# Performance work log

Hardware: AMD Instinct MI355X
Metric: run time of the kernel (lower is better)

The kernel has to match this reference:

```python
import jax, jax.numpy as jnp
import numpy as np

B, S, E, H = 4, 2048, 1024, 16
D = E // H
EPS = 1e-6


def setup_inputs() -> dict:
    key = jax.random.key(0)
    ks = jax.random.split(key, 6)
    glorot = lambda k: jax.random.uniform(k, (E, E), jnp.float32,
                                          -np.sqrt(6.0 / (E + E)), np.sqrt(6.0 / (E + E)))
    return {
        "x": jax.random.normal(ks[0], (B, S, E), jnp.float32),
        "mask": jnp.zeros((B, 1, 1, S), jnp.float32),
        "Wq": glorot(ks[1]), "bq": jnp.zeros((E,), jnp.float32),
        "Wk": glorot(ks[2]), "bk": jnp.zeros((E,), jnp.float32),
        "Wv": glorot(ks[3]), "bv": jnp.zeros((E,), jnp.float32),
        "Wo": glorot(ks[4]), "bo": jnp.zeros((E,), jnp.float32),
        "gamma": jnp.ones((E,), jnp.float32),
        "beta": jnp.zeros((E,), jnp.float32),
    }


def _split_heads(t):
    # [B, S, E] -> [B, H, S, D]
    return t.reshape(B, S, H, D).transpose(0, 2, 1, 3)


def reference(x, mask, Wq, bq, Wk, bk, Wv, bv, Wo, bo, gamma, beta):
    q = _split_heads(x @ Wq + bq)
    k = _split_heads(x @ Wk + bk)
    v = _split_heads(x @ Wv + bv)
    # NOTE: original divides by sqrt(embedding_size), not sqrt(depth)
    scores = jnp.einsum("bhqd,bhkd->bhqk", q, k) / jnp.sqrt(jnp.float32(E))
    scores = scores + mask * (-1e9)
    attn = jax.nn.softmax(scores, axis=-1)
    ctx = jnp.einsum("bhqk,bhkd->bhqd", attn, v)
    ctx = ctx.transpose(0, 2, 1, 3).reshape(B, S, E)
    main_out = ctx @ Wo + bo
    # dropout is identity (is_training=False); residual is the raw input
    added = main_out + x
    mu = jnp.mean(added, axis=-1, keepdims=True)
    var = jnp.mean(jnp.square(added - mu), axis=-1, keepdims=True)
    return gamma * (added - mu) / jnp.sqrt(var + EPS) + beta
```

## Files before the change

### kernel.cpp

```cpp
#include <hip/hip_runtime.h>
#include <hip/hip_bf16.h>


typedef __bf16 bf16_t;
typedef __bf16 bf16x8 __attribute__((ext_vector_type(8)));
typedef __bf16 bf16x4v __attribute__((ext_vector_type(4)));
typedef float f32x4 __attribute__((ext_vector_type(4)));

#define LDS_AS __attribute__((address_space(3)))
#define GLB_AS __attribute__((address_space(1)))

__device__ __forceinline__ void async16(bf16_t* lds, const bf16_t* g) {
  __builtin_amdgcn_global_load_lds((GLB_AS void*)const_cast<bf16_t*>(g),
                                   (LDS_AS void*)lds, 16, 0, 0);
}

__device__ __forceinline__ f32x4 mfma16(bf16x8 a, bf16x8 b, f32x4 c) {
  return __builtin_amdgcn_mfma_f32_16x16x32_bf16(a, b, c, 0, 0, 0);
}

__device__ __forceinline__ float fast_exp2(float x) {
#if __has_builtin(__builtin_amdgcn_exp2f)
  return __builtin_amdgcn_exp2f(x);
#else
  return __expf(x * 0.6931471805599453f);
#endif
}

__global__ __launch_bounds__(256) void prep_k(
    const float* __restrict__ w0, const float* __restrict__ w1,
    const float* __restrict__ w2, const float* __restrict__ w3,
    bf16_t* __restrict__ dst,
    const float* __restrict__ x, bf16_t* __restrict__ xb)
{
  const int tx = threadIdx.x, ty = threadIdx.y;
  if (blockIdx.z == 4) {
    const int id = (blockIdx.y * 32 + blockIdx.x) * 256 + ty * 32 + tx;
#pragma unroll
    for (int it = 0; it < 8; ++it) {
      const size_t i = ((size_t)id + (size_t)it * 262144) * 4;
      const float4 v = *(const float4*)(x + i);
      bf16x4v o;
      o[0] = (bf16_t)v.x; o[1] = (bf16_t)v.y; o[2] = (bf16_t)v.z; o[3] = (bf16_t)v.w;
      *(bf16x4v*)(xb + i) = o;
    }
    return;
  }
  __shared__ bf16_t tile[32][33];
  const float* src = (blockIdx.z == 0) ? w0 : (blockIdx.z == 1) ? w1
                   : (blockIdx.z == 2) ? w2 : w3;
  bf16_t* d = dst + (size_t)blockIdx.z * 1024 * 1024;
  const int bx = blockIdx.x * 32, by = blockIdx.y * 32;
#pragma unroll
  for (int r = 0; r < 32; r += 8)
    tile[ty + r][tx] = (bf16_t)src[(size_t)(by + ty + r) * 1024 + bx + tx];
  __syncthreads();
#pragma unroll
  for (int r = 0; r < 32; r += 8)
    d[(size_t)(bx + ty + r) * 1024 + by + tx] = tile[tx][ty + r];
}

__global__ __launch_bounds__(256) void gemm_qkv(
    const bf16_t* __restrict__ X, const bf16_t* __restrict__ WtAll,
    const float* __restrict__ bq, const float* __restrict__ bk,
    const float* __restrict__ bv,
    bf16_t* __restrict__ Qb, bf16_t* __restrict__ Kb, bf16_t* __restrict__ Vtb)
{
  __shared__ __align__(16) bf16_t As[128 * 64];
  __shared__ __align__(16) bf16_t Bs[128 * 64];

  const int z = blockIdx.z;
  const bf16_t* Bt = WtAll + (size_t)z * 1024 * 1024;
  const float* bias = (z == 0) ? bq : (z == 1) ? bk : bv;
  const int bm0 = blockIdx.x * 128;
  const int bn0 = blockIdx.y * 128;
  const int t = threadIdx.x;
  const int w = t >> 6, lane = t & 63;
  const int wm = w >> 1, wn = w & 1;
  const int l15 = lane & 15, quad = lane >> 4;
  const int srow8 = lane >> 3;
  const int sp8   = lane & 7;

  f32x4 acc[4][4] = {};

  for (int k0 = 0; k0 < 1024; k0 += 64) {
    __syncthreads();
#pragma unroll
    for (int i = 0; i < 4; ++i) {
      const int row = (w * 4 + i) * 8 + srow8;
      const int c = sp8 ^ (row & 7);
      async16(&As[row * 64 + sp8 * 8], X  + (size_t)(bm0 + row) * 1024 + k0 + c * 8);
      async16(&Bs[row * 64 + sp8 * 8], Bt + (size_t)(bn0 + row) * 1024 + k0 + c * 8);
    }
    __syncthreads();

    bf16x8 af[4][2], bfr[4][2];
#pragma unroll
    for (int mi = 0; mi < 4; ++mi) {
      const int r = wm * 64 + mi * 16 + l15;
#pragma unroll
      for (int kc = 0; kc < 2; ++kc) {
        const int pg = (kc * 4 + quad) ^ (r & 7);
        af[mi][kc] = *(const bf16x8*)&As[r * 64 + pg * 8];
      }
    }
#pragma unroll
    for (int ni = 0; ni < 4; ++ni) {
      const int r = wn * 64 + ni * 16 + l15;
#pragma unroll
      for (int kc = 0; kc < 2; ++kc) {
        const int pg = (kc * 4 + quad) ^ (r & 7);
        bfr[ni][kc] = *(const bf16x8*)&Bs[r * 64 + pg * 8];
      }
    }
#pragma unroll
    for (int kc = 0; kc < 2; ++kc)
#pragma unroll
      for (int mi = 0; mi < 4; ++mi)
#pragma unroll
        for (int ni = 0; ni < 4; ++ni)
          acc[mi][ni] = mfma16(af[mi][kc], bfr[ni][kc], acc[mi][ni]);
  }

  const float QSCALE = 0.045084220f;

#pragma unroll
  for (int ni = 0; ni < 4; ++ni) {
    const int n = bn0 + wn * 64 + ni * 16 + l15;
    const float bb = bias[n];
    const int h = n >> 6, dd = n & 63;
    if (z == 2) {
#pragma unroll
      for (int mi = 0; mi < 4; ++mi) {
        const int m0 = bm0 + wm * 64 + mi * 16 + quad * 4;
        const int bi = m0 >> 11, s = m0 & 2047;
        bf16x4v vk;
#pragma unroll
        for (int r = 0; r < 4; ++r) vk[r] = (bf16_t)(acc[mi][ni][r] + bb);
        *(bf16x4v*)&Vtb[((size_t)(bi * 16 + h) * 64 + dd) * 2048 + s] = vk;
      }
    } else {
#pragma unroll
      for (int mi = 0; mi < 4; ++mi) {
#pragma unroll
        for (int r = 0; r < 4; ++r) {
          const int m = bm0 + wm * 64 + mi * 16 + quad * 4 + r;
          const float v = acc[mi][ni][r] + bb;
          const int bi = m >> 11, s = m & 2047;
          if (z == 0)
            Qb[((size_t)(bi * 16 + h) * 2048 + s) * 64 + dd] = (bf16_t)(v * QSCALE);
          else
            Kb[((size_t)(bi * 16 + h) * 2048 + s) * 64 + dd] = (bf16_t)v;
        }
      }
    }
  }
}

__global__ __launch_bounds__(256) void attn_k(
    const bf16_t* __restrict__ Qb, const bf16_t* __restrict__ Kb,
    const bf16_t* __restrict__ Vtb, const float* __restrict__ mask,
    bf16_t* __restrict__ Ctx)
{
  __shared__ __align__(16) bf16_t Ks[2][64 * 64];
  __shared__ __align__(16) bf16_t Vs[2][64 * 64];
  __shared__ __align__(16) bf16_t Ps[256 * 64];

  const int qt = blockIdx.x, bh = blockIdx.y;
  const int bi = bh >> 4, h = bh & 15;
  const int q0 = qt * 256;
  const bf16_t* Qh = Qb + (size_t)bh * 2048 * 64;
  const bf16_t* Kh = Kb + (size_t)bh * 2048 * 64;
  const bf16_t* Vh = Vtb + (size_t)bh * 64 * 2048;
  const float* mrow = mask + (size_t)bi * 2048;

  const int t = threadIdx.x;
  const int w = t >> 6, lane = t & 63;
  const int l15 = lane & 15, quad = lane >> 4;
  const int srow = lane >> 3;
  const int sp = lane & 7;

  bf16x8 qb[4][2];
#pragma unroll
  for (int ni = 0; ni < 4; ++ni)
#pragma unroll
    for (int kc = 0; kc < 2; ++kc)
      qb[ni][kc] = *(const bf16x8*)&Qh[(size_t)(q0 + w * 64 + ni * 16 + l15) * 64
                                       + kc * 32 + quad * 8];

  bf16x8 ones;
#pragma unroll
  for (int i = 0; i < 8; ++i) ones[i] = (bf16_t)1.0f;

  f32x4 oacc[4][4] = {};
  f32x4 lacc[4] = {};

#pragma unroll
  for (int i = 0; i < 2; ++i) {
    const int row = (w * 2 + i) * 8 + srow;
    const int c = sp ^ (row & 7);
    async16(&Ks[0][row * 64 + sp * 8], Kh + (size_t)row * 64 + c * 8);
    async16(&Vs[0][row * 64 + sp * 8], Vh + (size_t)row * 2048 + c * 8);
  }
  __syncthreads();

#define ATTN_STEP(J, KC, VC, KN, VN, PREF)                                     \
  do {                                                                         \
    const int k0_ = (J) * 64;                                                  \
    if (PREF) {                                                                \
      const int k1_ = k0_ + 64;                                                \
      _Pragma("unroll")                                                        \
      for (int i = 0; i < 2; ++i) {                                            \
        const int row = (w * 2 + i) * 8 + srow;                                \
        const int c = sp ^ (row & 7);                                          \
        async16(&(KN)[row * 64 + sp * 8], Kh + (size_t)(k1_ + row) * 64 + c * 8); \
        async16(&(VN)[row * 64 + sp * 8], Vh + (size_t)row * 2048 + k1_ + c * 8); \
      }                                                                        \
    }                                                                          \
      \
    f32x4 sacc[4][4];                                                          \
    const float4* m4_ = (const float4*)(mrow + k0_);                           \
    _Pragma("unroll")                                                          \
    for (int mi = 0; mi < 4; ++mi) {                                           \
      const float4 mk = m4_[mi * 4 + quad];                                    \
      f32x4 ci;                                                                \
      ci[0] = mk.x * (-1.442695e9f);                                           \
      ci[1] = mk.y * (-1.442695e9f);                                           \
      ci[2] = mk.z * (-1.442695e9f);                                           \
      ci[3] = mk.w * (-1.442695e9f);                                           \
      _Pragma("unroll")                                                        \
      for (int ni = 0; ni < 4; ++ni) sacc[mi][ni] = ci;                        \
    }                                                                          \
    _Pragma("unroll")                                                          \
    for (int mi = 0; mi < 4; ++mi) {                                           \
      const int r = mi * 16 + l15;                                             \
      const bf16x8 kf0 = *(const bf16x8*)&(KC)[r * 64 + ((0 * 4 + quad) ^ (r & 7)) * 8]; \
      const bf16x8 kf1 = *(const bf16x8*)&(KC)[r * 64 + ((1 * 4 + quad) ^ (r & 7)) * 8]; \
      _Pragma("unroll")                                                        \
      for (int ni = 0; ni < 4; ++ni) {                                         \
        sacc[mi][ni] = mfma16(kf0, qb[ni][0], sacc[mi][ni]);                   \
        sacc[mi][ni] = mfma16(kf1, qb[ni][1], sacc[mi][ni]);                   \
      }                                                                        \
    }                                                                          \
                  \
    _Pragma("unroll")                                                          \
    for (int ni = 0; ni < 4; ++ni) {                                           \
      const int row = w * 64 + ni * 16 + l15;                                  \
      _Pragma("unroll")                                                        \
      for (int mi = 0; mi < 4; ++mi) {                                         \
        bf16x4v pk;                                                            \
        pk[0] = (bf16_t)fast_exp2(sacc[mi][ni][0]);                            \
        pk[1] = (bf16_t)fast_exp2(sacc[mi][ni][1]);                            \
        pk[2] = (bf16_t)fast_exp2(sacc[mi][ni][2]);                            \
        pk[3] = (bf16_t)fast_exp2(sacc[mi][ni][3]);                            \
        const int pg = (mi * 2 + (quad >> 1)) ^ (row & 7);                     \
        *(bf16x4v*)&Ps[row * 64 + pg * 8 + (quad & 1) * 4] = pk;               \
      }                                                                        \
    }                                                                          \
                  \
    bf16x8 pb[4][2];                                                           \
    _Pragma("unroll")                                                          \
    for (int ni = 0; ni < 4; ++ni)                                             \
      _Pragma("unroll")                                                        \
      for (int kc = 0; kc < 2; ++kc) {                                         \
        const int row = w * 64 + ni * 16 + l15;                                \
        const int pg = (kc * 4 + quad) ^ (row & 7);                            \
        pb[ni][kc] = *(const bf16x8*)&Ps[row * 64 + pg * 8];                   \
      }                                                                        \
    _Pragma("unroll")                                                          \
    for (int mi = 0; mi < 4; ++mi) {                                           \
      const int r = mi * 16 + l15;                                             \
      const bf16x8 av0 = *(const bf16x8*)&(VC)[r * 64 + ((0 * 4 + quad) ^ (r & 7)) * 8]; \
      const bf16x8 av1 = *(const bf16x8*)&(VC)[r * 64 + ((1 * 4 + quad) ^ (r & 7)) * 8]; \
      _Pragma("unroll")                                                        \
      for (int ni = 0; ni < 4; ++ni) {                                         \
        oacc[mi][ni] = mfma16(av0, pb[ni][0], oacc[mi][ni]);                   \
        oacc[mi][ni] = mfma16(av1, pb[ni][1], oacc[mi][ni]);                   \
      }                                                                        \
    }                                                                          \
    _Pragma("unroll")                                                          \
    for (int ni = 0; ni < 4; ++ni) {                                           \
      lacc[ni] = mfma16(ones, pb[ni][0], lacc[ni]);                            \
      lacc[ni] = mfma16(ones, pb[ni][1], lacc[ni]);                            \
    }                                                                          \
    __syncthreads();                                                           \
  } while (0)

  for (int jj = 0; jj < 16; ++jj) {
    ATTN_STEP(2 * jj,     Ks[0], Vs[0], Ks[1], Vs[1], true);
    ATTN_STEP(2 * jj + 1, Ks[1], Vs[1], Ks[0], Vs[0], jj < 15);
  }
#undef ATTN_STEP

#pragma unroll
  for (int ni = 0; ni < 4; ++ni) {
    const float inv = 1.0f / lacc[ni][0];
    const int s = q0 + w * 64 + ni * 16 + l15;
#pragma unroll
    for (int mi = 0; mi < 4; ++mi) {
      bf16x4v o4;
      o4[0] = (bf16_t)(oacc[mi][ni][0] * inv);
      o4[1] = (bf16_t)(oacc[mi][ni][1] * inv);
      o4[2] = (bf16_t)(oacc[mi][ni][2] * inv);
      o4[3] = (bf16_t)(oacc[mi][ni][3] * inv);
      *(bf16x4v*)&Ctx[((size_t)bi * 2048 + s) * 1024 + h * 64 + mi * 16 + quad * 4] = o4;
    }
  }
}

__global__ __launch_bounds__(256) void gemm_proj(
    const bf16_t* __restrict__ Ctx, const bf16_t* __restrict__ WoT,
    const float* __restrict__ bo, const float* __restrict__ Xres,
    float* __restrict__ Add)
{
  __shared__ __align__(16) bf16_t As[128 * 64];
  __shared__ __align__(16) bf16_t Bs[128 * 64];

  const int bm0 = blockIdx.x * 128;
  const int bn0 = blockIdx.y * 128;
  const int t = threadIdx.x;
  const int w = t >> 6, lane = t & 63;
  const int wm = w >> 1, wn = w & 1;
  const int l15 = lane & 15, quad = lane >> 4;
  const int srow8 = lane >> 3;
  const int sp8   = lane & 7;

  f32x4 acc[4][4] = {};

  for (int k0 = 0; k0 < 1024; k0 += 64) {
    __syncthreads();
#pragma unroll
    for (int i = 0; i < 4; ++i) {
      const int row = (w * 4 + i) * 8 + srow8;
      const int c = sp8 ^ (row & 7);
      async16(&As[row * 64 + sp8 * 8], Ctx + (size_t)(bm0 + row) * 1024 + k0 + c * 8);
      async16(&Bs[row * 64 + sp8 * 8], WoT + (size_t)(bn0 + row) * 1024 + k0 + c * 8);
    }
    __syncthreads();

    bf16x8 af[4][2], bfr[4][2];
#pragma unroll
    for (int mi = 0; mi < 4; ++mi) {
      const int r = wm * 64 + mi * 16 + l15;
#pragma unroll
      for (int kc = 0; kc < 2; ++kc) {
        const int pg = (kc * 4 + quad) ^ (r & 7);
        af[mi][kc] = *(const bf16x8*)&As[r * 64 + pg * 8];
      }
    }
#pragma unroll
    for (int ni = 0; ni < 4; ++ni) {
      const int r = wn * 64 + ni * 16 + l15;
#pragma unroll
      for (int kc = 0; kc < 2; ++kc) {
        const int pg = (kc * 4 + quad) ^ (r & 7);
        bfr[ni][kc] = *(const bf16x8*)&Bs[r * 64 + pg * 8];
      }
    }
#pragma unroll
    for (int kc = 0; kc < 2; ++kc)
#pragma unroll
      for (int mi = 0; mi < 4; ++mi)
#pragma unroll
        for (int ni = 0; ni < 4; ++ni)
          acc[mi][ni] = mfma16(af[mi][kc], bfr[ni][kc], acc[mi][ni]);
  }

#pragma unroll
  for (int ni = 0; ni < 4; ++ni) {
    const int n = bn0 + wn * 64 + ni * 16 + l15;
    const float bb = bo[n];
#pragma unroll
    for (int mi = 0; mi < 4; ++mi) {
#pragma unroll
      for (int r = 0; r < 4; ++r) {
        const int m = bm0 + wm * 64 + mi * 16 + quad * 4 + r;
        Add[(size_t)m * 1024 + n] =
            acc[mi][ni][r] + bb + Xres[(size_t)m * 1024 + n];
      }
    }
  }
}

__global__ __launch_bounds__(256) void ln_k(
    const float* __restrict__ A, const float* __restrict__ gamma,
    const float* __restrict__ beta, float* __restrict__ out)
{
  const int wid = threadIdx.x >> 6, lane = threadIdx.x & 63;
  const int row = blockIdx.x * 4 + wid;
  const float* a = A + (size_t)row * 1024;

  float4 v[4];
#pragma unroll
  for (int k = 0; k < 4; ++k) v[k] = ((const float4*)a)[lane + k * 64];

  float s = 0.f;
#pragma unroll
  for (int k = 0; k < 4; ++k) s += (v[k].x + v[k].y) + (v[k].z + v[k].w);
#pragma unroll
  for (int o = 1; o < 64; o <<= 1) s += __shfl_xor(s, o);
  const float mu = s * (1.0f / 1024.0f);

  float q = 0.f;
#pragma unroll
  for (int k = 0; k < 4; ++k) {
    v[k].x -= mu; v[k].y -= mu; v[k].z -= mu; v[k].w -= mu;
    q += (v[k].x * v[k].x + v[k].y * v[k].y) + (v[k].z * v[k].z + v[k].w * v[k].w);
  }
#pragma unroll
  for (int o = 1; o < 64; o <<= 1) q += __shfl_xor(q, o);
  const float rs = rsqrtf(q * (1.0f / 1024.0f) + 1e-6f);

#pragma unroll
  for (int k = 0; k < 4; ++k) {
    const int c = lane + k * 64;
    const float4 g4 = ((const float4*)gamma)[c];
    const float4 b4 = ((const float4*)beta)[c];
    float4 o4;
    o4.x = g4.x * v[k].x * rs + b4.x;
    o4.y = g4.y * v[k].y * rs + b4.y;
    o4.z = g4.z * v[k].z * rs + b4.z;
    o4.w = g4.w * v[k].w * rs + b4.w;
    ((float4*)(out + (size_t)row * 1024))[c] = o4;
  }
}

extern "C" void kernel_launch(void* const* d_in, const int* in_sizes, int n_in,
                              void* d_out, int out_size, void* d_ws, size_t ws_size,
                              hipStream_t stream)
{
  const float* x     = (const float*)d_in[0];
  const float* mask  = (const float*)d_in[1];
  const float* Wq    = (const float*)d_in[2];
  const float* bq    = (const float*)d_in[3];
  const float* Wk    = (const float*)d_in[4];
  const float* bk    = (const float*)d_in[5];
  const float* Wv    = (const float*)d_in[6];
  const float* bv    = (const float*)d_in[7];
  const float* Wo    = (const float*)d_in[8];
  const float* bo    = (const float*)d_in[9];
  const float* gamma = (const float*)d_in[10];
  const float* beta  = (const float*)d_in[11];
  float* out = (float*)d_out;

  bf16_t* Wt  = (bf16_t*)d_ws;
  bf16_t* Xb  = Wt + (size_t)4 * 1024 * 1024;
  bf16_t* Qb  = Xb + (size_t)8192 * 1024;
  bf16_t* Kb  = Qb + (size_t)8192 * 1024;
  bf16_t* Vtb = Kb + (size_t)8192 * 1024;
  bf16_t* Ctx = Vtb + (size_t)8192 * 1024;
  float*  Add = (float*)(Ctx + (size_t)8192 * 1024);

  prep_k<<<dim3(32, 32, 5), dim3(32, 8), 0, stream>>>(Wq, Wk, Wv, Wo, Wt, x, Xb);
  gemm_qkv<<<dim3(64, 8, 3), 256, 0, stream>>>(Xb, Wt, bq, bk, bv, Qb, Kb, Vtb);
  attn_k<<<dim3(8, 64), 256, 0, stream>>>(Qb, Kb, Vtb, mask, Ctx);
  gemm_proj<<<dim3(64, 8), 256, 0, stream>>>(Ctx, Wt + (size_t)3 * 1024 * 1024, bo, x, Add);
  ln_k<<<2048, 256, 0, stream>>>(Add, gamma, beta, out);
}
```

Baseline: 367.8 us.

## Stage pre-scaled mask in LDS, remap blocks across heads, add occupancy hint

```diff
diff --git a/kernel.cpp b/kernel.cpp
--- a/kernel.cpp
+++ b/kernel.cpp
@@ -157,16 +157,21 @@
   }
 }
 
-__global__ __launch_bounds__(256) void attn_k(
+__global__ __launch_bounds__(256, 4) void attn_k(
     const bf16_t* __restrict__ Qb, const bf16_t* __restrict__ Kb,
     const bf16_t* __restrict__ Vtb, const float* __restrict__ mask,
     bf16_t* __restrict__ Ctx)
 {
-  __shared__ __align__(16) bf16_t Ks[2][64 * 64];
-  __shared__ __align__(16) bf16_t Vs[2][64 * 64];
+  __shared__ __align__(16) bf16_t Ks0[64 * 64];
+  __shared__ __align__(16) bf16_t Ks1[64 * 64];
+  __shared__ __align__(16) bf16_t Vs0[64 * 64];
+  __shared__ __align__(16) bf16_t Vs1[64 * 64];
   __shared__ __align__(16) bf16_t Ps[256 * 64];
-
-  const int qt = blockIdx.x, bh = blockIdx.y;
+  __shared__ __align__(16) bf16_t maskb[2048];
+
+  const int lin = blockIdx.y * 8 + blockIdx.x;
+  const int qt = lin >> 6;
+  const int bh = (lin & 7) * 8 + ((lin >> 3) & 7);
   const int bi = bh >> 4, h = bh & 15;
   const int q0 = qt * 256;
   const bf16_t* Qh = Qb + (size_t)bh * 2048 * 64;
@@ -180,6 +185,18 @@
   const int srow = lane >> 3;
   const int sp = lane & 7;
 
+#pragma unroll
+  for (int it = 0; it < 2; ++it) {
+    const int idx = (it * 256 + t) * 4;
+    const float4 mv = *(const float4*)(mrow + idx);
+    bf16x4v mb;
+    mb[0] = (bf16_t)(mv.x * (-1.442695e9f));
+    mb[1] = (bf16_t)(mv.y * (-1.442695e9f));
+    mb[2] = (bf16_t)(mv.z * (-1.442695e9f));
+    mb[3] = (bf16_t)(mv.w * (-1.442695e9f));
+    *(bf16x4v*)&maskb[idx] = mb;
+  }
+
   bf16x8 qb[4][2];
 #pragma unroll
   for (int ni = 0; ni < 4; ++ni)
@@ -199,8 +216,8 @@
   for (int i = 0; i < 2; ++i) {
     const int row = (w * 2 + i) * 8 + srow;
     const int c = sp ^ (row & 7);
-    async16(&Ks[0][row * 64 + sp * 8], Kh + (size_t)row * 64 + c * 8);
-    async16(&Vs[0][row * 64 + sp * 8], Vh + (size_t)row * 2048 + c * 8);
+    async16(&Ks0[row * 64 + sp * 8], Kh + (size_t)row * 64 + c * 8);
+    async16(&Vs0[row * 64 + sp * 8], Vh + (size_t)row * 2048 + c * 8);
   }
   __syncthreads();
 
@@ -217,17 +234,14 @@
         async16(&(VN)[row * 64 + sp * 8], Vh + (size_t)row * 2048 + k1_ + c * 8); \
       }                                                                        \
     }                                                                          \
-      \
+          \
     f32x4 sacc[4][4];                                                          \
-    const float4* m4_ = (const float4*)(mrow + k0_);                           \
     _Pragma("unroll")                                                          \
     for (int mi = 0; mi < 4; ++mi) {                                           \
-      const float4 mk = m4_[mi * 4 + quad];                                    \
+      const bf16x4v mb = *(const bf16x4v*)&maskb[k0_ + mi * 16 + quad * 4];    \
       f32x4 ci;                                                                \
-      ci[0] = mk.x * (-1.442695e9f);                                           \
-      ci[1] = mk.y * (-1.442695e9f);                                           \
-      ci[2] = mk.z * (-1.442695e9f);                                           \
-      ci[3] = mk.w * (-1.442695e9f);                                           \
+      ci[0] = (float)mb[0]; ci[1] = (float)mb[1];                              \
+      ci[2] = (float)mb[2]; ci[3] = (float)mb[3];                              \
       _Pragma("unroll")                                                        \
       for (int ni = 0; ni < 4; ++ni) sacc[mi][ni] = ci;                        \
     }                                                                          \
@@ -287,8 +301,8 @@
   } while (0)
 
   for (int jj = 0; jj < 16; ++jj) {
-    ATTN_STEP(2 * jj,     Ks[0], Vs[0], Ks[1], Vs[1], true);
-    ATTN_STEP(2 * jj + 1, Ks[1], Vs[1], Ks[0], Vs[0], jj < 15);
+    ATTN_STEP(2 * jj,     Ks0, Vs0, Ks1, Vs1, true);
+    ATTN_STEP(2 * jj + 1, Ks1, Vs1, Ks0, Vs0, jj < 15);
   }
 #undef ATTN_STEP
 
```

After: 323.9 us. 11.9% less time.
